# Optimization experiments

Measured on AMD Instinct MI355X. Metric: run time of the kernel, lower is better.

Reference implementation:

```python
import jax, jax.numpy as jnp
from jax import lax
import numpy as np

BETA = 0.9   # snn.Leaky(beta=0.9)
THR = 1.0    # snntorch default threshold, reset_mechanism='subtract'

@jax.custom_vjp
def spike(x):
    return (x > 0.0).astype(x.dtype)

def _spike_fwd(x):
    return spike(x), x

def _spike_bwd(x, g):
    # snntorch surrogate.atan (alpha=2): dS/dx = 1 / (1 + (pi*x)^2)
    return (g / (1.0 + (jnp.pi * x) ** 2),)

spike.defvjp(_spike_fwd, _spike_bwd)

def lif(inp, mem):
    # snntorch Leaky: reset based on PREVIOUS mem, detached; subtract mechanism
    reset = lax.stop_gradient(spike(mem - THR))
    mem = BETA * mem + inp - reset * THR
    return spike(mem - THR), mem

def conv1d(x, w, b):
    # x: (B, Cin, L), w: (Cout, Cin, K), VALID padding
    y = lax.conv_general_dilated(x, w, window_strides=(1,), padding='VALID',
                                 dimension_numbers=('NCH', 'OIH', 'NCH'))
    return y + b[None, :, None]

def setup_inputs() -> dict:
    key = jax.random.key(0)
    ks = jax.random.split(key, 11)
    B, L, T, num_c = 1024, 30, 100, 10
    def init(k, shape, fan_in):
        bound = 1.0 / np.sqrt(fan_in)
        return jax.random.uniform(k, shape, jnp.float32, -bound, bound)
    return {
        'x':   jax.random.normal(ks[0], (B, 1, L, T), jnp.float32),
        'w1':  init(ks[1], (16, 1, 7), 1 * 7),   'b1': init(ks[2], (16,), 7),
        'w2':  init(ks[3], (32, 16, 5), 16 * 5), 'b2': init(ks[4], (32,), 80),
        'w3':  init(ks[5], (64, 32, 3), 32 * 3), 'b3': init(ks[6], (64,), 96),
        'fw1': init(ks[7], (256, 64 * 18), 64 * 18), 'fb1': init(ks[8], (256,), 64 * 18),
        'fw2': init(ks[9], (num_c, 256), 256),       'fb2': init(ks[10], (num_c,), 256),
    }

def reference(x, w1, b1, w2, b2, w3, b3, fw1, fb1, fw2, fb2):
    B = x.shape[0]
    num_c = fw2.shape[0]
    xt_seq = jnp.transpose(x, (3, 0, 1, 2))  # (T, B, 1, 30)
    mems = (jnp.zeros((B, 16, 24), x.dtype),  # after conv1 (k=7): 30->24
            jnp.zeros((B, 32, 20), x.dtype),  # after conv2 (k=5): 24->20
            jnp.zeros((B, 64, 18), x.dtype),  # after conv3 (k=3): 20->18
            jnp.zeros((B, 256), x.dtype),
            jnp.zeros((B, num_c), x.dtype))
    def step(mems, xt):
        m1, m2, m3, m4, m5 = mems
        h = conv1d(xt, w1, b1); s, m1 = lif(h, m1)
        h = conv1d(s, w2, b2);  s, m2 = lif(h, m2)
        h = conv1d(s, w3, b3);  s, m3 = lif(h, m3)
        h = s.reshape(B, -1) @ fw1.T + fb1; s, m4 = lif(h, m4)
        h = s @ fw2.T + fb2;               s, m5 = lif(h, m5)
        return (m1, m2, m3, m4, m5), s
    _, spk_rec = lax.scan(step, mems, xt_seq)
    return spk_rec  # (T, B, num_c) -- matches torch.stack(spk_rec)
```

## Files before the change

kernel.cpp:

```cpp
#include <hip/hip_runtime.h>
#include <stdint.h>

#define BETA 0.9f

__global__ void transpose_fw1(const float* __restrict__ A, float* __restrict__ At) {
    __shared__ float tile[32][33];
    const int i0 = blockIdx.x * 32;
    const int j0 = blockIdx.y * 32;
    const int tx = threadIdx.x, ty = threadIdx.y;
    for (int r = ty; r < 32; r += 8)
        tile[r][tx] = A[(j0 + r) * 1152 + i0 + tx];
    __syncthreads();
    for (int r = ty; r < 32; r += 8)
        At[(i0 + r) * 256 + j0 + tx] = tile[tx][r];
}

__global__ __launch_bounds__(768)
__attribute__((amdgpu_waves_per_eu(6)))
void snn_main(
    const float* __restrict__ x,
    const float* __restrict__ w1, const float* __restrict__ b1,
    const float* __restrict__ w2, const float* __restrict__ b2,
    const float* __restrict__ w3, const float* __restrict__ b3,
    const float* __restrict__ fw1T,
    const float* __restrict__ fb1,
    const float* __restrict__ fw2, const float* __restrict__ fb2,
    float* __restrict__ out)
{
    const int b    = blockIdx.x;
    const int tid  = threadIdx.x;
    const int e    = (tid >= 384) ? 1 : 0;
    const int tl   = tid - 384 * e;
    const int lane = tid & 63;
    const int ew   = tl >> 6;

    __shared__ float w2L[16 * 5 * 32];
    __shared__ float w3L[32 * 3 * 64];
    __shared__ float pacc[2][6][256];
    __shared__ float s1e[2][16 * 24 + 8];
    __shared__ float s4[2][256];
    __shared__ unsigned long long masks[2][18];
    __shared__ unsigned int rm1[2][2][16];
    __shared__ unsigned int cm2[2][2][20];

    const int c1 = tl & 15;
    const int l1 = tl >> 4;
    const int c2 = tl & 31;
    const int g2 = tl >> 5;
    const int l02 = 2 * g2;
    const bool c2on = (g2 < 10);
    const unsigned wmask2 = c2on ? (0x3Fu << l02) : 0u;
    const int c3 = lane;
    const int l03 = ew * 3;

    for (int i = tid; i < 16 * 5 * 32; i += 768) {
        const int cc = i & 31, r = i >> 5;
        w2L[i] = w2[cc * 80 + r];
    }
    for (int i = tid; i < 32 * 3 * 64; i += 768) {
        const int cc = i & 63, r = i >> 6;
        w3L[i] = w3[cc * 96 + r];
    }
    if (tl < 16) { rm1[e][0][tl] = 0u; rm1[e][1][tl] = 0u; }
    if (tl < 20) { cm2[e][0][tl] = 0u; cm2[e][1][tl] = 0u; }
    if (tl < 8)  s1e[e][384 + tl] = 0.0f;

    float w1r[7];
#pragma unroll
    for (int k = 0; k < 7; ++k) w1r[k] = w1[c1 * 7 + k];
    const float b1r = b1[c1];
    const float b2r = b2[c2];
    const float b3r = b3[c3];
    const float fb1r = (tl < 256) ? fb1[tl] : 0.0f;
    const int jf = tl >> 4, chf = tl & 15;
    const float fb2r = (tl < 160 && chf == 0) ? fb2[jf] : 0.0f;

    float m1 = 0.f;
    float m2[2] = {0.f, 0.f};
    float m3[3] = {0.f, 0.f, 0.f};
    float m4 = 0.f, m5 = 0.f;

    const float* xb = x + (2 * b + e) * 3000;
    const int out_b = (2 * b + e) * 10;
    const float4* fw1Tv = reinterpret_cast<const float4*>(fw1T);

    float xr[7];
#pragma unroll
    for (int k = 0; k < 7; ++k) xr[k] = xb[(l1 + k) * 100];

    __syncthreads();

    {
        float h = b1r;
#pragma unroll
        for (int k = 0; k < 7; ++k) h += xr[k] * w1r[k];
        float rs = (m1 > 1.0f) ? 1.0f : 0.0f;
        m1 = BETA * m1 + h - rs;
        float sa = (m1 > 1.0f) ? 1.0f : 0.0f;
        s1e[e][c1 * 24 + l1] = sa;
        if (sa != 0.0f) atomicOr(&rm1[e][0][c1], 1u << l1);
    }
    __syncthreads();

    for (int t = 0; t < 100; ++t) {
        const int pb = t & 1, pn = pb ^ 1;

        {
            if (tl < 16) rm1[e][pn][tl] = 0u;
            if (tl < 20) cm2[e][pn][tl] = 0u;
            if (t < 99) {
#pragma unroll
                for (int k = 0; k < 7; ++k) xr[k] = xb[(l1 + k) * 100 + t + 1];
            }
            float h[2] = {b2r, b2r};
#pragma unroll
            for (int ci = 0; ci < 16; ++ci) {
                const unsigned rmv =
                    __builtin_amdgcn_readfirstlane(rm1[e][pb][ci]);
                if ((rmv & wmask2) == 0u) continue;
                const float2* wp2 =
                    (const float2*)&s1e[e][ci * 24 + l02];
                const float2 wa = wp2[0], wb = wp2[1], wc = wp2[2];
                float wk[5];
#pragma unroll
                for (int k = 0; k < 5; ++k) wk[k] = w2L[(ci * 5 + k) * 32 + c2];
                h[0] += wa.x * wk[0]; h[0] += wa.y * wk[1];
                h[0] += wb.x * wk[2]; h[0] += wb.y * wk[3];
                h[0] += wc.x * wk[4];
                h[1] += wa.y * wk[0]; h[1] += wb.x * wk[1];
                h[1] += wb.y * wk[2]; h[1] += wc.x * wk[3];
                h[1] += wc.y * wk[4];
            }
            if (c2on) {
#pragma unroll
                for (int li = 0; li < 2; ++li) {
                    float rs = (m2[li] > 1.0f) ? 1.0f : 0.0f;
                    m2[li] = BETA * m2[li] + h[li] - rs;
                    if (m2[li] > 1.0f) atomicOr(&cm2[e][pb][l02 + li], 1u << c2);
                }
            }
        }
        __syncthreads();

        {
            float h[3] = {b3r, b3r, b3r};
#pragma unroll
            for (int wl = 0; wl < 5; ++wl) {
                unsigned cm = __builtin_amdgcn_readfirstlane(cm2[e][pb][l03 + wl]);
                while (cm) {
                    const int ci = (int)__builtin_ctz(cm); cm &= cm - 1;
                    const float* wp = &w3L[ci * 192 + c3];
#pragma unroll
                    for (int k = 0; k < 3; ++k) {
                        const int li = wl - k;
                        if (li >= 0 && li < 3)
                            h[li] += wp[k * 64];
                    }
                }
            }
#pragma unroll
            for (int li = 0; li < 3; ++li) {
                float rs = (m3[li] > 1.0f) ? 1.0f : 0.0f;
                m3[li] = BETA * m3[li] + h[li] - rs;
                float s = (m3[li] > 1.0f) ? 1.0f : 0.0f;
                unsigned long long mk = __ballot(s != 0.0f);
                if (lane == 0) masks[e][l03 + li] = mk;
            }
        }
        __syncthreads();

        if (t < 99) {
            float h = b1r;
#pragma unroll
            for (int k = 0; k < 7; ++k) h += xr[k] * w1r[k];
            float rs = (m1 > 1.0f) ? 1.0f : 0.0f;
            m1 = BETA * m1 + h - rs;
            float sa = (m1 > 1.0f) ? 1.0f : 0.0f;
            s1e[e][c1 * 24 + l1] = sa;
            if (sa != 0.0f) atomicOr(&rm1[e][pn][c1], 1u << l1);
        }

        {
            float4 acc4; acc4.x = acc4.y = acc4.z = acc4.w = 0.0f;
#pragma unroll 1
            for (int l = ew; l < 18; l += 6) {
                const unsigned* mp = (const unsigned*)&masks[e][l];
                const unsigned mlo = __builtin_amdgcn_readfirstlane(mp[0]);
                const unsigned mhi = __builtin_amdgcn_readfirstlane(mp[1]);
                unsigned long long mk = ((unsigned long long)mhi << 32) | mlo;
                while (mk) {
                    float4 f0, f1, f2, f3;
                    f0.x=f0.y=f0.z=f0.w=0.f; f1=f0; f2=f0; f3=f0;
                    int c;
                    c = (int)__builtin_ctzll(mk); mk &= mk - 1;
                    f0 = fw1Tv[(c * 18 + l) * 64 + lane];
                    if (mk) { c = (int)__builtin_ctzll(mk); mk &= mk - 1;
                              f1 = fw1Tv[(c * 18 + l) * 64 + lane]; }
                    if (mk) { c = (int)__builtin_ctzll(mk); mk &= mk - 1;
                              f2 = fw1Tv[(c * 18 + l) * 64 + lane]; }
                    if (mk) { c = (int)__builtin_ctzll(mk); mk &= mk - 1;
                              f3 = fw1Tv[(c * 18 + l) * 64 + lane]; }
                    acc4.x += f0.x; acc4.y += f0.y; acc4.z += f0.z; acc4.w += f0.w;
                    acc4.x += f1.x; acc4.y += f1.y; acc4.z += f1.z; acc4.w += f1.w;
                    acc4.x += f2.x; acc4.y += f2.y; acc4.z += f2.z; acc4.w += f2.w;
                    acc4.x += f3.x; acc4.y += f3.y; acc4.z += f3.z; acc4.w += f3.w;
                }
            }
            ((float4*)&pacc[e][ew][0])[lane] = acc4;
        }
        __syncthreads();

        if (tl < 256) {
            float acc = fb1r;
#pragma unroll
            for (int w = 0; w < 6; ++w) acc += pacc[e][w][tl];
            float rs = (m4 > 1.0f) ? 1.0f : 0.0f;
            m4 = BETA * m4 + acc - rs;
            s4[e][tl] = (m4 > 1.0f) ? 1.0f : 0.0f;
        }
        __syncthreads();

        if (tl < 160) {
            const float* wrow = fw2 + jf * 256;
            float p = 0.f;
#pragma unroll
            for (int i = 0; i < 16; ++i)
                p += s4[e][i * 16 + chf] * wrow[i * 16 + chf];
            p += __shfl_xor(p, 8, 16);
            p += __shfl_xor(p, 4, 16);
            p += __shfl_xor(p, 2, 16);
            p += __shfl_xor(p, 1, 16);
            if (chf == 0) {
                float h = fb2r + p;
                float rs = (m5 > 1.0f) ? 1.0f : 0.0f;
                m5 = BETA * m5 + h - rs;
                out[t * 10240 + out_b + jf] = (m5 > 1.0f) ? 1.0f : 0.0f;
            }
        }
    }
}

extern "C" void kernel_launch(void* const* d_in, const int* in_sizes, int n_in,
                              void* d_out, int out_size, void* d_ws, size_t ws_size,
                              hipStream_t stream) {
    const float* x   = (const float*)d_in[0];
    const float* w1  = (const float*)d_in[1];
    const float* b1  = (const float*)d_in[2];
    const float* w2  = (const float*)d_in[3];
    const float* b2  = (const float*)d_in[4];
    const float* w3  = (const float*)d_in[5];
    const float* b3  = (const float*)d_in[6];
    const float* fw1 = (const float*)d_in[7];
    const float* fb1 = (const float*)d_in[8];
    const float* fw2 = (const float*)d_in[9];
    const float* fb2 = (const float*)d_in[10];
    float* out  = (float*)d_out;
    float* fw1T = (float*)d_ws;

    dim3 tb(32, 8);
    dim3 tg(1152 / 32, 256 / 32);
    transpose_fw1<<<tg, tb, 0, stream>>>(fw1, fw1T);
    snn_main<<<512, 768, 0, stream>>>(x, w1, b1, w2, b2, w3, b3,
                                      fw1T, fb1, fw2, fb2, out);
}
```

Baseline: 622.0 us.

## Software-pipeline SNN layers across timesteps to cut barriers per step

```diff
diff --git a/kernel.cpp b/kernel.cpp
--- a/kernel.cpp
+++ b/kernel.cpp
@@ -37,7 +37,7 @@
     __shared__ float w2L[16 * 5 * 32];
     __shared__ float w3L[32 * 3 * 64];
     __shared__ float pacc[2][6][256];
-    __shared__ float s1e[2][16 * 24 + 8];
+    __shared__ float s1e[2][2][16 * 24 + 8];
     __shared__ float s4[2][256];
     __shared__ unsigned long long masks[2][18];
     __shared__ unsigned int rm1[2][2][16];
@@ -63,7 +63,7 @@
     }
     if (tl < 16) { rm1[e][0][tl] = 0u; rm1[e][1][tl] = 0u; }
     if (tl < 20) { cm2[e][0][tl] = 0u; cm2[e][1][tl] = 0u; }
-    if (tl < 8)  s1e[e][384 + tl] = 0.0f;
+    if (tl < 8)  { s1e[e][0][384 + tl] = 0.0f; s1e[e][1][384 + tl] = 0.0f; }
 
     float w1r[7];
 #pragma unroll
@@ -97,29 +97,90 @@
         float rs = (m1 > 1.0f) ? 1.0f : 0.0f;
         m1 = BETA * m1 + h - rs;
         float sa = (m1 > 1.0f) ? 1.0f : 0.0f;
-        s1e[e][c1 * 24 + l1] = sa;
+        s1e[e][0][c1 * 24 + l1] = sa;
         if (sa != 0.0f) atomicOr(&rm1[e][0][c1], 1u << l1);
+#pragma unroll
+        for (int k = 0; k < 7; ++k) xr[k] = xb[(l1 + k) * 100 + 1];
+    }
+    __syncthreads();
+    {
+        float h[2] = {b2r, b2r};
+#pragma unroll
+        for (int ci = 0; ci < 16; ++ci) {
+            const unsigned rmv = __builtin_amdgcn_readfirstlane(rm1[e][0][ci]);
+            if ((rmv & wmask2) == 0u) continue;
+            const float2* wp2 = (const float2*)&s1e[e][0][ci * 24 + l02];
+            const float2 wa = wp2[0], wb = wp2[1], wc = wp2[2];
+            float wk[5];
+#pragma unroll
+            for (int k = 0; k < 5; ++k) wk[k] = w2L[(ci * 5 + k) * 32 + c2];
+            h[0] += wa.x * wk[0]; h[0] += wa.y * wk[1];
+            h[0] += wb.x * wk[2]; h[0] += wb.y * wk[3];
+            h[0] += wc.x * wk[4];
+            h[1] += wa.y * wk[0]; h[1] += wb.x * wk[1];
+            h[1] += wb.y * wk[2]; h[1] += wc.x * wk[3];
+            h[1] += wc.y * wk[4];
+        }
+        if (c2on) {
+#pragma unroll
+            for (int li = 0; li < 2; ++li) {
+                float rs = (m2[li] > 1.0f) ? 1.0f : 0.0f;
+                m2[li] = BETA * m2[li] + h[li] - rs;
+                if (m2[li] > 1.0f) atomicOr(&cm2[e][0][l02 + li], 1u << c2);
+            }
+        }
+        float h1 = b1r;
+#pragma unroll
+        for (int k = 0; k < 7; ++k) h1 += xr[k] * w1r[k];
+        float rs = (m1 > 1.0f) ? 1.0f : 0.0f;
+        m1 = BETA * m1 + h1 - rs;
+        float sa = (m1 > 1.0f) ? 1.0f : 0.0f;
+        s1e[e][1][c1 * 24 + l1] = sa;
+        if (sa != 0.0f) atomicOr(&rm1[e][1][c1], 1u << l1);
+    }
+    __syncthreads();
+    {
+        float h[3] = {b3r, b3r, b3r};
+#pragma unroll
+        for (int wl = 0; wl < 5; ++wl) {
+            unsigned cm = __builtin_amdgcn_readfirstlane(cm2[e][0][l03 + wl]);
+            while (cm) {
+                const int ci = (int)__builtin_ctz(cm); cm &= cm - 1;
+                const float* wp = &w3L[ci * 192 + c3];
+#pragma unroll
+                for (int k = 0; k < 3; ++k) {
+                    const int li = wl - k;
+                    if (li >= 0 && li < 3) h[li] += wp[k * 64];
+                }
+            }
+        }
+#pragma unroll
+        for (int li = 0; li < 3; ++li) {
+            float rs = (m3[li] > 1.0f) ? 1.0f : 0.0f;
+            m3[li] = BETA * m3[li] + h[li] - rs;
+            float s = (m3[li] > 1.0f) ? 1.0f : 0.0f;
+            unsigned long long mk = __ballot(s != 0.0f);
+            if (lane == 0) masks[e][l03 + li] = mk;
+        }
     }
     __syncthreads();
 
     for (int t = 0; t < 100; ++t) {
-        const int pb = t & 1, pn = pb ^ 1;
-
-        {
-            if (tl < 16) rm1[e][pn][tl] = 0u;
-            if (tl < 20) cm2[e][pn][tl] = 0u;
-            if (t < 99) {
-#pragma unroll
-                for (int k = 0; k < 7; ++k) xr[k] = xb[(l1 + k) * 100 + t + 1];
-            }
+        const int pi = t & 1;
+        const int pc = pi ^ 1;
+
+        if (t < 98) {
+#pragma unroll
+            for (int k = 0; k < 7; ++k) xr[k] = xb[(l1 + k) * 100 + t + 2];
+        }
+        if (t < 99) {
             float h[2] = {b2r, b2r};
 #pragma unroll
             for (int ci = 0; ci < 16; ++ci) {
                 const unsigned rmv =
-                    __builtin_amdgcn_readfirstlane(rm1[e][pb][ci]);
+                    __builtin_amdgcn_readfirstlane(rm1[e][pc][ci]);
                 if ((rmv & wmask2) == 0u) continue;
-                const float2* wp2 =
-                    (const float2*)&s1e[e][ci * 24 + l02];
+                const float2* wp2 = (const float2*)&s1e[e][pc][ci * 24 + l02];
                 const float2 wa = wp2[0], wb = wp2[1], wc = wp2[2];
                 float wk[5];
 #pragma unroll
@@ -136,50 +197,10 @@
                 for (int li = 0; li < 2; ++li) {
                     float rs = (m2[li] > 1.0f) ? 1.0f : 0.0f;
                     m2[li] = BETA * m2[li] + h[li] - rs;
-                    if (m2[li] > 1.0f) atomicOr(&cm2[e][pb][l02 + li], 1u << c2);
+                    if (m2[li] > 1.0f) atomicOr(&cm2[e][pc][l02 + li], 1u << c2);
                 }
             }
         }
-        __syncthreads();
-
-        {
-            float h[3] = {b3r, b3r, b3r};
-#pragma unroll
-            for (int wl = 0; wl < 5; ++wl) {
-                unsigned cm = __builtin_amdgcn_readfirstlane(cm2[e][pb][l03 + wl]);
-                while (cm) {
-                    const int ci = (int)__builtin_ctz(cm); cm &= cm - 1;
-                    const float* wp = &w3L[ci * 192 + c3];
-#pragma unroll
-                    for (int k = 0; k < 3; ++k) {
-                        const int li = wl - k;
-                        if (li >= 0 && li < 3)
-                            h[li] += wp[k * 64];
-                    }
-                }
-            }
-#pragma unroll
-            for (int li = 0; li < 3; ++li) {
-                float rs = (m3[li] > 1.0f) ? 1.0f : 0.0f;
-                m3[li] = BETA * m3[li] + h[li] - rs;
-                float s = (m3[li] > 1.0f) ? 1.0f : 0.0f;
-                unsigned long long mk = __ballot(s != 0.0f);
-                if (lane == 0) masks[e][l03 + li] = mk;
-            }
-        }
-        __syncthreads();
-
-        if (t < 99) {
-            float h = b1r;
-#pragma unroll
-            for (int k = 0; k < 7; ++k) h += xr[k] * w1r[k];
-            float rs = (m1 > 1.0f) ? 1.0f : 0.0f;
-            m1 = BETA * m1 + h - rs;
-            float sa = (m1 > 1.0f) ? 1.0f : 0.0f;
-            s1e[e][c1 * 24 + l1] = sa;
-            if (sa != 0.0f) atomicOr(&rm1[e][pn][c1], 1u << l1);
-        }
-
         {
             float4 acc4; acc4.x = acc4.y = acc4.z = acc4.w = 0.0f;
 #pragma unroll 1
@@ -210,6 +231,33 @@
         }
         __syncthreads();
 
+        if (tl < 16) rm1[e][pi][tl] = 0u;
+        if (tl < 20) cm2[e][pi][tl] = 0u;
+        if (t < 99) {
+            float h[3] = {b3r, b3r, b3r};
+#pragma unroll
+            for (int wl = 0; wl < 5; ++wl) {
+                unsigned cm =
+                    __builtin_amdgcn_readfirstlane(cm2[e][pc][l03 + wl]);
+                while (cm) {
+                    const int ci = (int)__builtin_ctz(cm); cm &= cm - 1;
+                    const float* wp = &w3L[ci * 192 + c3];
+#pragma unroll
+                    for (int k = 0; k < 3; ++k) {
+                        const int li = wl - k;
+                        if (li >= 0 && li < 3) h[li] += wp[k * 64];
+                    }
+                }
+            }
+#pragma unroll
+            for (int li = 0; li < 3; ++li) {
+                float rs = (m3[li] > 1.0f) ? 1.0f : 0.0f;
+                m3[li] = BETA * m3[li] + h[li] - rs;
+                float s = (m3[li] > 1.0f) ? 1.0f : 0.0f;
+                unsigned long long mk = __ballot(s != 0.0f);
+                if (lane == 0) masks[e][l03 + li] = mk;
+            }
+        }
         if (tl < 256) {
             float acc = fb1r;
 #pragma unroll
@@ -237,6 +285,17 @@
                 out[t * 10240 + out_b + jf] = (m5 > 1.0f) ? 1.0f : 0.0f;
             }
         }
+        if (t < 98) {
+            float h = b1r;
+#pragma unroll
+            for (int k = 0; k < 7; ++k) h += xr[k] * w1r[k];
+            float rs = (m1 > 1.0f) ? 1.0f : 0.0f;
+            m1 = BETA * m1 + h - rs;
+            float sa = (m1 > 1.0f) ? 1.0f : 0.0f;
+            s1e[e][pi][c1 * 24 + l1] = sa;
+            if (sa != 0.0f) atomicOr(&rm1[e][pi][c1], 1u << l1);
+        }
+        __syncthreads();
     }
 }
 
```

Result: no change. 624.4 us (+0.4%).
